# Performance work log

Hardware: AMD Instinct MI355X
Metric: run time of the kernel (lower is better)

Reference implementation:

```python
import jax, jax.numpy as jnp
import numpy as np

MAX_M = 16


def _twiddle(n, m):
    # exp(-2i*pi*n_a*m_a / (n*m)), shape (n, m), precomputed on host (static n, m)
    a = np.outer(np.arange(n), np.arange(m))
    return jnp.asarray(np.exp(-2j * np.pi * a / (n * m)).astype(np.complex64))


def _ref_dft_real(n, H):
    # reference DFT matrix as (H, n, n, 2) real view, matching ref_dft_matrix
    a = np.outer(np.arange(n), np.arange(n))
    M = np.exp(-2j * np.pi * a / n).astype(np.complex64)  # (n, n)
    M = np.broadcast_to(M, (H, n, n))
    return jnp.asarray(np.stack([M.real, M.imag], axis=-1).astype(np.float32))


def _cooley_tukey(k, n, m, mats):
    # k: (..., H, n*m) complex; mats[p]: (H, p, p) complex
    k = k.reshape(*k.shape[:-1], m, n)                      # (..., H, m, n)
    kf = jnp.einsum('hmo,...hon->...hmn', mats[m], k)       # m-length DFTs
    kf = jnp.einsum('nm,...mn->...nm', _twiddle(n, m), kf)  # twiddle + transpose -> (..., H, n, m)
    if n <= MAX_M:
        kf = jnp.einsum('hno,...hom->...hnm', mats[n], kf)  # n-length DFTs
    else:
        kf = jnp.moveaxis(kf, -1, -3)                        # '... h n m -> ... m h n'
        kf = _cooley_tukey(kf, n // MAX_M, MAX_M, mats)
        kf = jnp.moveaxis(kf, -3, -1)                        # '... m h n -> ... h n m'
    return kf.reshape(*kf.shape[:-2], n * m)


def block_fft(x, N, mats):
    # x: (..., H, L) complex, zero-pad to N, then recursive block FFT
    L = x.shape[-1]
    if L != N:
        x = jnp.pad(x, [(0, 0)] * (x.ndim - 1) + [(0, N - L)])
    return _cooley_tukey(x, N // MAX_M, MAX_M, mats)


def block_ifft(x, N, mats):
    return jnp.conj(block_fft(jnp.conj(x), N, mats)) / N


def setup_inputs() -> dict:
    key = jax.random.key(0)
    B, H, L = 16, 512, 1024
    ku, kk, kd = jax.random.split(key, 3)
    u = jax.random.normal(ku, (B, H, L), dtype=jnp.float32)
    k = jax.random.normal(kk, (H, L), dtype=jnp.float32) / L
    D = jax.random.normal(kd, (H,), dtype=jnp.float32)
    return {
        'u': u, 'k': k, 'D': D,
        'mat_2': _ref_dft_real(2, H),
        'mat_4': _ref_dft_real(4, H),
        'mat_8': _ref_dft_real(8, H),
        'mat_16': _ref_dft_real(16, H),
    }


def reference(u, k, D, mat_2, mat_4, mat_8, mat_16):
    cplx = lambda m: (m[..., 0] + 1j * m[..., 1]).astype(jnp.complex64)
    mats = {2: cplx(mat_2), 4: cplx(mat_4), 8: cplx(mat_8), 16: cplx(mat_16)}
    L = u.shape[-1]
    N = 2 * L  # causal FFT conv length
    k_f = block_fft(k.astype(jnp.complex64), N, mats)   # (H, N)
    u_f = block_fft(u.astype(jnp.complex64), N, mats)   # (B, H, N)
    y = block_ifft(u_f * k_f, N, mats)[..., :L].real    # (B, H, L)
    return (y + u * D[:, None]).astype(jnp.float32)
```

## Files before the change

kernel.cpp:

```cpp
#include <hip/hip_runtime.h>
#include <math.h>

#define NT     128
#define NB     16
#define NH     512
#define SEQ_L  1024
#define FFT_N  2048
#define RS     0.70710678118654752f
#define C16    0.92387953251128675f
#define S16    0.38268343236508977f

typedef float f2 __attribute__((ext_vector_type(2)));

__device__ __forceinline__ f2 in_(f2 v) { return (f2){v.y, -v.x}; }
__device__ __forceinline__ f2 ip_(f2 v) { return (f2){-v.y, v.x}; }
__device__ __forceinline__ f2 cmul(f2 a, f2 b) {
    return a.x * b + a.y * (f2){-b.y, b.x};
}
__device__ __forceinline__ f2 cmulj(f2 a, f2 b) {
    return b.x * a + b.y * (f2){a.y, -a.x};
}

#define BUF2_SZ 2176

__device__ __align__(16) float4 g_kf4[(size_t)NH * (FFT_N / 2)];

template <int SIGN>
__device__ __forceinline__ void dft4(f2 x[4]) {
    f2 s0 = x[0] + x[2], s1 = x[0] - x[2];
    f2 s2 = x[1] + x[3], s3 = x[1] - x[3];
    x[0] = s0 + s2;
    x[2] = s0 - s2;
    if (SIGN < 0) { x[1] = s1 + in_(s3); x[3] = s1 + ip_(s3); }
    else          { x[1] = s1 + ip_(s3); x[3] = s1 + in_(s3); }
}

template <int SIGN>
__device__ __forceinline__ void dft8(f2 x[8]) {
    f2 e0 = x[0] + x[4], e1 = x[1] + x[5];
    f2 e2 = x[2] + x[6], e3 = x[3] + x[7];
    f2 o0 = x[0] - x[4], o1 = x[1] - x[5];
    f2 o2 = x[2] - x[6], o3 = x[3] - x[7];
    f2 t1, t2, t3;
    if (SIGN < 0) {
        t1 = RS * (o1 + in_(o1));
        t2 = in_(o2);
        t3 = -RS * (o3 + ip_(o3));
    } else {
        t1 = RS * (o1 + ip_(o1));
        t2 = ip_(o2);
        t3 = -RS * (o3 + in_(o3));
    }
    f2 s0 = e0 + e2, s1 = e0 - e2, s2 = e1 + e3, s3 = e1 - e3;
    x[0] = s0 + s2;
    x[4] = s0 - s2;
    f2 u0 = o0 + t2, u1 = o0 - t2, u2 = t1 + t3, u3 = t1 - t3;
    x[1] = u0 + u2;
    x[5] = u0 - u2;
    if (SIGN < 0) {
        x[2] = s1 + in_(s3); x[6] = s1 + ip_(s3);
        x[3] = u1 + in_(u3); x[7] = u1 + ip_(u3);
    } else {
        x[2] = s1 + ip_(s3); x[6] = s1 + in_(s3);
        x[3] = u1 + ip_(u3); x[7] = u1 + in_(u3);
    }
}

template <int SIGN>
__device__ __forceinline__ void dft16_twiddle(f2 v[4][4]) {
    const float sg = (SIGN < 0) ? -1.f : 1.f;
    const f2 W1 = (f2){C16, sg * S16};
    const f2 W2 = (f2){RS, sg * RS};
    const f2 W3 = (f2){S16, sg * C16};
    const f2 W6 = (f2){-RS, sg * RS};
    const f2 W9 = (f2){-C16, -sg * S16};
    v[1][1] = cmul(v[1][1], W1);
    v[1][2] = cmul(v[1][2], W2);
    v[1][3] = cmul(v[1][3], W3);
    v[2][1] = cmul(v[2][1], W2);
    v[2][2] = (SIGN < 0) ? in_(v[2][2]) : ip_(v[2][2]);
    v[2][3] = cmul(v[2][3], W6);
    v[3][1] = cmul(v[3][1], W3);
    v[3][2] = cmul(v[3][2], W6);
    v[3][3] = cmul(v[3][3], W9);
}

template <int SIGN>
__device__ __forceinline__ void dft16(f2 x[16]) {
    f2 v[4][4];
#pragma unroll
    for (int n0 = 0; n0 < 4; ++n0) {
        f2 a[4] = {x[n0], x[n0 + 4], x[n0 + 8], x[n0 + 12]};
        dft4<SIGN>(a);
        v[n0][0] = a[0]; v[n0][1] = a[1]; v[n0][2] = a[2]; v[n0][3] = a[3];
    }
    dft16_twiddle<SIGN>(v);
#pragma unroll
    for (int k0 = 0; k0 < 4; ++k0) {
        f2 a[4] = {v[0][k0], v[1][k0], v[2][k0], v[3][k0]};
        dft4<SIGN>(a);
        x[k0] = a[0]; x[k0 + 4] = a[1]; x[k0 + 8] = a[2]; x[k0 + 12] = a[3];
    }
}

__device__ __forceinline__ void dft16_zero8(const f2 z[8], f2 x[16]) {
    f2 v[4][4];
#pragma unroll
    for (int n0 = 0; n0 < 4; ++n0) {
        f2 a = z[n0], b = z[n0 + 4];
        v[n0][0] = a + b;
        v[n0][1] = a + in_(b);
        v[n0][2] = a - b;
        v[n0][3] = a + ip_(b);
    }
    dft16_twiddle<-1>(v);
#pragma unroll
    for (int k0 = 0; k0 < 4; ++k0) {
        f2 a[4] = {v[0][k0], v[1][k0], v[2][k0], v[3][k0]};
        dft4<-1>(a);
        x[k0] = a[0]; x[k0 + 4] = a[1]; x[k0 + 8] = a[2]; x[k0 + 12] = a[3];
    }
}

__device__ __forceinline__ void dft16_inv_low8(const f2 x[16], f2 y[8]) {
    f2 v[4][4];
#pragma unroll
    for (int n0 = 0; n0 < 4; ++n0) {
        f2 a[4] = {x[n0], x[n0 + 4], x[n0 + 8], x[n0 + 12]};
        dft4<+1>(a);
        v[n0][0] = a[0]; v[n0][1] = a[1]; v[n0][2] = a[2]; v[n0][3] = a[3];
    }
    dft16_twiddle<+1>(v);
#pragma unroll
    for (int k0 = 0; k0 < 4; ++k0) {
        f2 x0 = v[0][k0], x1 = v[1][k0], x2 = v[2][k0], x3 = v[3][k0];
        f2 s0 = x0 + x2, s1 = x0 - x2;
        f2 s2 = x1 + x3, s3 = x1 - x3;
        y[k0]     = s0 + s2;
        y[k0 + 4] = s1 + ip_(s3);
    }
}

template <int CONJ>
__device__ __forceinline__ void tw_apply16(f2 x[16], f2 a) {
#define AP(v, w) (v) = CONJ ? cmulj((v), (w)) : cmul((v), (w))
    AP(x[1], a);
    f2 w2 = cmul(a, a);      AP(x[2], w2);
    f2 w3 = cmul(w2, a);     AP(x[3], w3);
    f2 w4 = cmul(w2, w2);    AP(x[4], w4);
    f2 w5 = cmul(w4, a);     AP(x[5], w5);
    f2 w6 = cmul(w4, w2);    AP(x[6], w6);
    f2 w7 = cmul(w6, a);     AP(x[7], w7);
    f2 w8 = cmul(w4, w4);    AP(x[8], w8);
    f2 w9 = cmul(w8, a);     AP(x[9], w9);
    f2 w10 = cmul(w8, w2);   AP(x[10], w10);
    f2 w11 = cmul(w10, a);   AP(x[11], w11);
    f2 w12 = cmul(w8, w4);   AP(x[12], w12);
    f2 w13 = cmul(w12, a);   AP(x[13], w13);
    f2 w14 = cmul(w12, w2);  AP(x[14], w14);
    f2 w15 = cmul(w14, a);   AP(x[15], w15);
#undef AP
}

__global__ __launch_bounds__(NT, 2) void kfft_kernel(const float* __restrict__ kin) {
    __shared__ f2 buf[BUF2_SZ];
    __shared__ f2 twlds[NT];
    const int t = threadIdx.x;
    const int h = blockIdx.x;
    f2 w1;
    {
        float sv, cv;
        sincosf(-6.283185307179586f * (float)t / (float)FFT_N, &sv, &cv);
        w1 = (f2){cv, sv};
        twlds[t] = w1;
    }
    const int pb1 = t + (t >> 4);
    const float* krow = kin + (size_t)h * SEQ_L;
    {
        f2 z[8], x[16];
#pragma unroll
        for (int j = 0; j < 8; ++j) z[j] = (f2){krow[t + 128 * j], 0.f};
        dft16_zero8(z, x);
        tw_apply16<0>(x, w1);
#pragma unroll
        for (int c = 0; c < 16; ++c) buf[pb1 + 136 * c] = x[c];
    }
    __syncthreads();
    const int cblk = t >> 3, r = t & 7;
    const int pb2 = 136 * cblk + r;
    {
        f2 x[16];
#pragma unroll
        for (int j = 0; j < 16; ++j) x[j] = buf[pb2 + 8 * j + (j >> 1)];
        dft16<-1>(x);
        tw_apply16<0>(x, twlds[16 * r]);
#pragma unroll
        for (int c2 = 0; c2 < 16; ++c2) buf[pb2 + 8 * c2 + (c2 >> 1)] = x[c2];
    }
    __syncthreads();
    const int pb3 = 17 * t;
    float4* kf4 = g_kf4 + (size_t)h * (FFT_N / 2);
#pragma unroll
    for (int gi = 0; gi < 2; ++gi) {
        f2 x[8];
#pragma unroll
        for (int l = 0; l < 8; ++l) x[l] = buf[pb3 + 8 * gi + l];
        dft8<-1>(x);
#pragma unroll
        for (int q = 0; q < 4; ++q)
            kf4[(4 * gi + q) * 128 + t] =
                make_float4(x[2 * q].x, x[2 * q].y, x[2 * q + 1].x, x[2 * q + 1].y);
    }
}

__global__ __launch_bounds__(NT, 2) void conv_pair_kernel(const float* __restrict__ u,
                                                          const float* __restrict__ D,
                                                          float* __restrict__ out) {
    __shared__ f2 buf[BUF2_SZ];
    __shared__ f2 twlds[NT];
    const int t = threadIdx.x;
    const int h = blockIdx.x & (NH - 1);
    const int bp = blockIdx.x >> 9;
    const size_t row0 = (size_t)(2 * bp) * NH + h;
    const size_t row1 = row0 + NH;
    const float* u0 = u + row0 * SEQ_L;
    const float* u1 = u + row1 * SEQ_L;
    f2 w1;
    {
        float sv, cv;
        sincosf(-6.283185307179586f * (float)t / (float)FFT_N, &sv, &cv);
        w1 = (f2){cv, sv};
        twlds[t] = w1;
    }
    const int pb1 = t + (t >> 4);
    f2 uz[8];
    {
        f2 x[16];
#pragma unroll
        for (int j = 0; j < 8; ++j)
            uz[j] = (f2){u0[t + 128 * j], u1[t + 128 * j]};
        dft16_zero8(uz, x);
        tw_apply16<0>(x, w1);
#pragma unroll
        for (int c = 0; c < 16; ++c) buf[pb1 + 136 * c] = x[c];
    }
    __syncthreads();
    const int cblk = t >> 3, r = t & 7;
    const int pb2 = 136 * cblk + r;
    const f2 ws = twlds[16 * r];
    {
        f2 x[16];
#pragma unroll
        for (int j = 0; j < 16; ++j) x[j] = buf[pb2 + 8 * j + (j >> 1)];
        dft16<-1>(x);
        tw_apply16<0>(x, ws);
#pragma unroll
        for (int c2 = 0; c2 < 16; ++c2) buf[pb2 + 8 * c2 + (c2 >> 1)] = x[c2];
    }
    __syncthreads();
    {
        const float4* kf4 = g_kf4 + (size_t)h * (FFT_N / 2);
        const int pb3 = 17 * t;
#pragma unroll
        for (int gi = 0; gi < 2; ++gi) {
            f2 x[8];
#pragma unroll
            for (int l = 0; l < 8; ++l) x[l] = buf[pb3 + 8 * gi + l];
            dft8<-1>(x);
#pragma unroll
            for (int q = 0; q < 4; ++q) {
                float4 kk = kf4[(4 * gi + q) * 128 + t];
                x[2 * q]     = cmul(x[2 * q],     (f2){kk.x, kk.y});
                x[2 * q + 1] = cmul(x[2 * q + 1], (f2){kk.z, kk.w});
            }
            dft8<+1>(x);
#pragma unroll
            for (int l = 0; l < 8; ++l) buf[pb3 + 8 * gi + l] = x[l];
        }
    }
    __syncthreads();
    {
        f2 x[16];
#pragma unroll
        for (int c2 = 0; c2 < 16; ++c2) x[c2] = buf[pb2 + 8 * c2 + (c2 >> 1)];
        tw_apply16<1>(x, ws);
        dft16<+1>(x);
#pragma unroll
        for (int j = 0; j < 16; ++j) buf[pb2 + 8 * j + (j >> 1)] = x[j];
    }
    __syncthreads();
    {
        f2 x[16];
#pragma unroll
        for (int c = 0; c < 16; ++c) x[c] = buf[pb1 + 136 * c];
        tw_apply16<1>(x, w1);
        f2 y[8];
        dft16_inv_low8(x, y);
        const float Dh = D[h];
        const float invN = 1.0f / (float)FFT_N;
        float* o0row = out + row0 * SEQ_L;
        float* o1row = out + row1 * SEQ_L;
#pragma unroll
        for (int j = 0; j < 8; ++j) {
            f2 o = y[j] * invN + uz[j] * Dh;
            o0row[t + 128 * j] = o.x;
            o1row[t + 128 * j] = o.y;
        }
    }
}

extern "C" void kernel_launch(void* const* d_in, const int* in_sizes, int n_in,
                              void* d_out, int out_size, void* d_ws, size_t ws_size,
                              hipStream_t stream) {
    const float* u = (const float*)d_in[0];
    const float* k = (const float*)d_in[1];
    const float* D = (const float*)d_in[2];
    float* out = (float*)d_out;

    kfft_kernel<<<NH, NT, 0, stream>>>(k);
    conv_pair_kernel<<<NB * NH / 2, NT, 0, stream>>>(u, D, out);
}
```

Baseline: 111.9 us.

## Process four batch rows per block, sharing kernel spectrum loads and twiddles

The conv kernel now handles two packed complex pairs (four batch rows) per block instead of one pair. Each block runs two interleaved FFT pipelines through two LDS buffers. This halves the grid size and amortizes the kernel-spectrum global loads, twiddle computation and barriers across twice the work, while exposing more independent ILP per thread. The costs are double the LDS footprint and higher register pressure, which could cut occupancy or cause spills. Fewer blocks may also leave CUs underused.

New measurement: 114.8 us. +2.6%, slower.

```diff
diff --git a/kernel.cpp b/kernel.cpp
--- a/kernel.cpp
+++ b/kernel.cpp
@@ -213,18 +213,27 @@
     }
 }
 
-__global__ __launch_bounds__(NT, 2) void conv_pair_kernel(const float* __restrict__ u,
+__global__ __launch_bounds__(NT, 2) void conv_quad_kernel(const float* __restrict__ u,
                                                           const float* __restrict__ D,
                                                           float* __restrict__ out) {
-    __shared__ f2 buf[BUF2_SZ];
+    __shared__ f2 bufA[BUF2_SZ];
+    __shared__ f2 bufB[BUF2_SZ];
     __shared__ f2 twlds[NT];
     const int t = threadIdx.x;
     const int h = blockIdx.x & (NH - 1);
-    const int bp = blockIdx.x >> 9;
-    const size_t row0 = (size_t)(2 * bp) * NH + h;
-    const size_t row1 = row0 + NH;
-    const float* u0 = u + row0 * SEQ_L;
-    const float* u1 = u + row1 * SEQ_L;
+    const int q = blockIdx.x >> 9;
+    const size_t rA0 = (size_t)(4 * q) * NH + h;
+    const float* uA0 = u + rA0 * SEQ_L;
+    const float* uA1 = uA0 + (size_t)NH * SEQ_L;
+    const float* uB0 = uA0 + (size_t)2 * NH * SEQ_L;
+    const float* uB1 = uA0 + (size_t)3 * NH * SEQ_L;
+
+    f2 uzA[8], uzB[8];
+#pragma unroll
+    for (int j = 0; j < 8; ++j) uzA[j] = (f2){uA0[t + 128 * j], uA1[t + 128 * j]};
+#pragma unroll
+    for (int j = 0; j < 8; ++j) uzB[j] = (f2){uB0[t + 128 * j], uB1[t + 128 * j]};
+
     f2 w1;
     {
         float sv, cv;
@@ -233,29 +242,36 @@
         twlds[t] = w1;
     }
     const int pb1 = t + (t >> 4);
-    f2 uz[8];
     {
         f2 x[16];
-#pragma unroll
-        for (int j = 0; j < 8; ++j)
-            uz[j] = (f2){u0[t + 128 * j], u1[t + 128 * j]};
-        dft16_zero8(uz, x);
+        dft16_zero8(uzA, x);
         tw_apply16<0>(x, w1);
 #pragma unroll
-        for (int c = 0; c < 16; ++c) buf[pb1 + 136 * c] = x[c];
+        for (int c = 0; c < 16; ++c) bufA[pb1 + 136 * c] = x[c];
+        f2 y[16];
+        dft16_zero8(uzB, y);
+        tw_apply16<0>(y, w1);
+#pragma unroll
+        for (int c = 0; c < 16; ++c) bufB[pb1 + 136 * c] = y[c];
     }
     __syncthreads();
     const int cblk = t >> 3, r = t & 7;
     const int pb2 = 136 * cblk + r;
     const f2 ws = twlds[16 * r];
     {
-        f2 x[16];
-#pragma unroll
-        for (int j = 0; j < 16; ++j) x[j] = buf[pb2 + 8 * j + (j >> 1)];
+        f2 x[16], y[16];
+#pragma unroll
+        for (int j = 0; j < 16; ++j) x[j] = bufA[pb2 + 8 * j + (j >> 1)];
+#pragma unroll
+        for (int j = 0; j < 16; ++j) y[j] = bufB[pb2 + 8 * j + (j >> 1)];
         dft16<-1>(x);
         tw_apply16<0>(x, ws);
 #pragma unroll
-        for (int c2 = 0; c2 < 16; ++c2) buf[pb2 + 8 * c2 + (c2 >> 1)] = x[c2];
+        for (int c2 = 0; c2 < 16; ++c2) bufA[pb2 + 8 * c2 + (c2 >> 1)] = x[c2];
+        dft16<-1>(y);
+        tw_apply16<0>(y, ws);
+#pragma unroll
+        for (int c2 = 0; c2 < 16; ++c2) bufB[pb2 + 8 * c2 + (c2 >> 1)] = y[c2];
     }
     __syncthreads();
     {
@@ -263,48 +279,84 @@
         const int pb3 = 17 * t;
 #pragma unroll
         for (int gi = 0; gi < 2; ++gi) {
-            f2 x[8];
-#pragma unroll
-            for (int l = 0; l < 8; ++l) x[l] = buf[pb3 + 8 * gi + l];
+            const float4 k0 = kf4[(4 * gi + 0) * 128 + t];
+            const float4 k1 = kf4[(4 * gi + 1) * 128 + t];
+            const float4 k2 = kf4[(4 * gi + 2) * 128 + t];
+            const float4 k3 = kf4[(4 * gi + 3) * 128 + t];
+            f2 x[8], y[8];
+#pragma unroll
+            for (int l = 0; l < 8; ++l) x[l] = bufA[pb3 + 8 * gi + l];
+#pragma unroll
+            for (int l = 0; l < 8; ++l) y[l] = bufB[pb3 + 8 * gi + l];
             dft8<-1>(x);
-#pragma unroll
-            for (int q = 0; q < 4; ++q) {
-                float4 kk = kf4[(4 * gi + q) * 128 + t];
-                x[2 * q]     = cmul(x[2 * q],     (f2){kk.x, kk.y});
-                x[2 * q + 1] = cmul(x[2 * q + 1], (f2){kk.z, kk.w});
-            }
+            x[0] = cmul(x[0], (f2){k0.x, k0.y});
+            x[1] = cmul(x[1], (f2){k0.z, k0.w});
+            x[2] = cmul(x[2], (f2){k1.x, k1.y});
+            x[3] = cmul(x[3], (f2){k1.z, k1.w});
+            x[4] = cmul(x[4], (f2){k2.x, k2.y});
+            x[5] = cmul(x[5], (f2){k2.z, k2.w});
+            x[6] = cmul(x[6], (f2){k3.x, k3.y});
+            x[7] = cmul(x[7], (f2){k3.z, k3.w});
             dft8<+1>(x);
 #pragma unroll
-            for (int l = 0; l < 8; ++l) buf[pb3 + 8 * gi + l] = x[l];
+            for (int l = 0; l < 8; ++l) bufA[pb3 + 8 * gi + l] = x[l];
+            dft8<-1>(y);
+            y[0] = cmul(y[0], (f2){k0.x, k0.y});
+            y[1] = cmul(y[1], (f2){k0.z, k0.w});
+            y[2] = cmul(y[2], (f2){k1.x, k1.y});
+            y[3] = cmul(y[3], (f2){k1.z, k1.w});
+            y[4] = cmul(y[4], (f2){k2.x, k2.y});
+            y[5] = cmul(y[5], (f2){k2.z, k2.w});
+            y[6] = cmul(y[6], (f2){k3.x, k3.y});
+            y[7] = cmul(y[7], (f2){k3.z, k3.w});
+            dft8<+1>(y);
+#pragma unroll
+            for (int l = 0; l < 8; ++l) bufB[pb3 + 8 * gi + l] = y[l];
         }
     }
     __syncthreads();
     {
-        f2 x[16];
-#pragma unroll
-        for (int c2 = 0; c2 < 16; ++c2) x[c2] = buf[pb2 + 8 * c2 + (c2 >> 1)];
+        f2 x[16], y[16];
+#pragma unroll
+        for (int c2 = 0; c2 < 16; ++c2) x[c2] = bufA[pb2 + 8 * c2 + (c2 >> 1)];
+#pragma unroll
+        for (int c2 = 0; c2 < 16; ++c2) y[c2] = bufB[pb2 + 8 * c2 + (c2 >> 1)];
         tw_apply16<1>(x, ws);
         dft16<+1>(x);
 #pragma unroll
-        for (int j = 0; j < 16; ++j) buf[pb2 + 8 * j + (j >> 1)] = x[j];
-    }
-    __syncthreads();
-    {
-        f2 x[16];
-#pragma unroll
-        for (int c = 0; c < 16; ++c) x[c] = buf[pb1 + 136 * c];
-        tw_apply16<1>(x, w1);
-        f2 y[8];
-        dft16_inv_low8(x, y);
+        for (int j = 0; j < 16; ++j) bufA[pb2 + 8 * j + (j >> 1)] = x[j];
+        tw_apply16<1>(y, ws);
+        dft16<+1>(y);
+#pragma unroll
+        for (int j = 0; j < 16; ++j) bufB[pb2 + 8 * j + (j >> 1)] = y[j];
+    }
+    __syncthreads();
+    {
         const float Dh = D[h];
         const float invN = 1.0f / (float)FFT_N;
-        float* o0row = out + row0 * SEQ_L;
-        float* o1row = out + row1 * SEQ_L;
+        f2 x[16], y[16];
+#pragma unroll
+        for (int c = 0; c < 16; ++c) x[c] = bufA[pb1 + 136 * c];
+#pragma unroll
+        for (int c = 0; c < 16; ++c) y[c] = bufB[pb1 + 136 * c];
+        tw_apply16<1>(x, w1);
+        f2 yA[8];
+        dft16_inv_low8(x, yA);
+        tw_apply16<1>(y, w1);
+        f2 yB[8];
+        dft16_inv_low8(y, yB);
+        float* oA0 = out + rA0 * SEQ_L;
+        float* oA1 = oA0 + (size_t)NH * SEQ_L;
+        float* oB0 = oA0 + (size_t)2 * NH * SEQ_L;
+        float* oB1 = oA0 + (size_t)3 * NH * SEQ_L;
 #pragma unroll
         for (int j = 0; j < 8; ++j) {
-            f2 o = y[j] * invN + uz[j] * Dh;
-            o0row[t + 128 * j] = o.x;
-            o1row[t + 128 * j] = o.y;
+            f2 oA = yA[j] * invN + uzA[j] * Dh;
+            f2 oB = yB[j] * invN + uzB[j] * Dh;
+            oA0[t + 128 * j] = oA.x;
+            oA1[t + 128 * j] = oA.y;
+            oB0[t + 128 * j] = oB.x;
+            oB1[t + 128 * j] = oB.y;
         }
     }
 }
@@ -318,5 +370,5 @@
     float* out = (float*)d_out;
 
     kfft_kernel<<<NH, NT, 0, stream>>>(k);
-    conv_pair_kernel<<<NB * NH / 2, NT, 0, stream>>>(u, D, out);
-}
+    conv_quad_kernel<<<NB * NH / 4, NT, 0, stream>>>(u, D, out);
+}
```
